# Kernel tuning notes

Hardware: AMD Instinct MI355X
Metric: run time of the kernel (lower is better)

## Reference

```python
import jax, jax.numpy as jnp
import numpy as np

EPS = 1e-5

def setup_inputs() -> dict:
    key = jax.random.key(0)
    ks = jax.random.split(key, 8)
    b, c, p, h = 8, 128, 2048, 4
    inp = {
        "input": jax.random.normal(ks[0], (b, c, p), jnp.float32),
        "gamma": jnp.ones((c,), jnp.float32),
        "beta": jnp.zeros((c,), jnp.float32),
        "Wq": jax.random.normal(ks[1], (c * h, c), jnp.float32) * (c ** -0.5),
        "bq": jnp.zeros((c * h,), jnp.float32),
        "Wk": jax.random.normal(ks[2], (c * h, c), jnp.float32) * (c ** -0.5),
        "bk": jnp.zeros((c * h,), jnp.float32),
        "Wv": jax.random.normal(ks[3], (c * h, c), jnp.float32) * (c ** -0.5),
        "bv": jnp.zeros((c * h,), jnp.float32),
        "Wo": jax.random.normal(ks[4], (c, c * h), jnp.float32) * ((c * h) ** -0.5),
        "bo": jnp.zeros((c,), jnp.float32),
    }
    return inp


def reference(input, gamma, beta, Wq, bq, Wk, bk, Wv, bv, Wo, bo):
    b, c, p = input.shape
    h = Wq.shape[0] // c
    # BatchNorm1d (training-mode batch stats): mean/var per channel over (batch, points)
    mean = jnp.mean(input, axis=(0, 2), keepdims=True)          # [1,c,1]
    var = jnp.mean((input - mean) ** 2, axis=(0, 2), keepdims=True)
    x = (input - mean) * jax.lax.rsqrt(var + EPS)
    x = x * gamma[None, :, None] + beta[None, :, None]
    # 1x1 conv projections == channel matmuls; then split c*h -> (c, h)
    q = (jnp.einsum('oc,bcp->bop', Wq, x) + bq[None, :, None]).reshape(b, c, h, p)
    k = (jnp.einsum('oc,bcp->bop', Wk, x) + bk[None, :, None]).reshape(b, c, h, p)
    v = (jnp.einsum('oc,bcp->bop', Wv, x) + bv[None, :, None]).reshape(b, c, h, p)
    # attention over points; scale by c**-0.5
    weight = jnp.einsum('bchi,bchj->bhij', q, k) * (c ** -0.5)   # [b,h,p,p]
    weight = jax.nn.softmax(weight, axis=3)
    att = jnp.einsum('bhij,bchj->bchi', weight, v)               # [b,c,h,p]
    att = att.reshape(b, c * h, p)
    out = jnp.einsum('oc,bcp->bop', Wo, att) + bo[None, :, None]
    return out + input
```

## Files before the change

### kernel.cpp

```cpp
#include <hip/hip_runtime.h>
#include <hip/hip_bf16.h>

#define NB 8
#define NC 128
#define NP 2048
#define NH 4
#define NCH 512

typedef __attribute__((ext_vector_type(8))) short bf16x8;
typedef __attribute__((ext_vector_type(16))) float f32x16;

__device__ __forceinline__ float bf2f(unsigned short u) {
  return __uint_as_float(((unsigned)u) << 16);
}
__device__ __forceinline__ unsigned short f2bf(float f) {
  __hip_bfloat16 h = __float2bfloat16(f);
  return *reinterpret_cast<unsigned short*>(&h);
}
__device__ __forceinline__ unsigned pk2(float lo, float hi) {
  return (unsigned)f2bf(lo) | ((unsigned)f2bf(hi) << 16);
}
__device__ __forceinline__ void gload_lds16(const void* g, void* l) {
  __builtin_amdgcn_global_load_lds(
      (const __attribute__((address_space(1))) void*)g,
      (__attribute__((address_space(3))) void*)l, 16, 0, 0);
}
__device__ __forceinline__ void plswap(unsigned& a, unsigned& b) {
  asm volatile("v_permlane32_swap_b32 %0, %1" : "+v"(a), "+v"(b));
}

__global__ __launch_bounds__(256) void bn_partial(
    const float* __restrict__ in, float* __restrict__ psum,
    float* __restrict__ psum2) {
  int c = blockIdx.x >> 2, qtr = blockIdx.x & 3;
  int t = threadIdx.x;
  float s = 0.f, s2 = 0.f;
  for (int b = 0; b < NB; ++b) {
    const float* ptr = in + ((size_t)b * NC + c) * NP + qtr * 512;
    #pragma unroll
    for (int p = 0; p < 2; ++p) {
      float v = ptr[p * 256 + t];
      s += v; s2 += v * v;
    }
  }
  for (int off = 32; off; off >>= 1) {
    s += __shfl_down(s, off, 64);
    s2 += __shfl_down(s2, off, 64);
  }
  __shared__ float red[8];
  int lane = t & 63, wid = t >> 6;
  if (!lane) { red[wid] = s; red[wid + 4] = s2; }
  __syncthreads();
  if (!t) {
    psum[blockIdx.x] = red[0] + red[1] + red[2] + red[3];
    psum2[blockIdx.x] = red[4] + red[5] + red[6] + red[7];
  }
}

__global__ __launch_bounds__(512, 2) void qkv_proj(
    const float* __restrict__ in, const float* __restrict__ gamma,
    const float* __restrict__ beta, const float* __restrict__ psum,
    const float* __restrict__ psum2, const float* __restrict__ Wq,
    const float* __restrict__ bq, const float* __restrict__ Wk,
    const float* __restrict__ bk, const float* __restrict__ Wv,
    const float* __restrict__ bv, unsigned short* __restrict__ qws,
    unsigned short* __restrict__ kws, unsigned short* __restrict__ vws) {
  __shared__ float sc[128], sh[128], bias[1536];
  __shared__ __align__(16) unsigned short Xt[64][136];
  int t = threadIdx.x;
  int pt = blockIdx.x & 31, b = blockIdx.x >> 5;
  int p0 = pt * 64;
  if (t < 128) {
    float s = psum[t * 4] + psum[t * 4 + 1] + psum[t * 4 + 2] + psum[t * 4 + 3];
    float s2 = psum2[t * 4] + psum2[t * 4 + 1] + psum2[t * 4 + 2] + psum2[t * 4 + 3];
    const float invn = 1.f / (NB * NP);
    float mean = s * invn, var = s2 * invn - mean * mean;
    float scl = gamma[t] * rsqrtf(var + 1e-5f);
    sc[t] = scl; sh[t] = beta[t] - mean * scl;
  }
  bias[t] = bq[t]; bias[512 + t] = bk[t]; bias[1024 + t] = bv[t];
  __syncthreads();
  {
    int p = t & 63, c0 = (t >> 6) * 16;
    const float* src = in + ((size_t)b * NC + c0) * NP + p0 + p;
    #pragma unroll
    for (int cc = 0; cc < 16; ++cc) {
      float v = src[(size_t)cc * NP];
      Xt[p][c0 + cc] = f2bf(v * sc[c0 + cc] + sh[c0 + cc]);
    }
  }
  __syncthreads();
  int w = t >> 6, lane = t & 63, l31 = lane & 31, h5 = lane >> 5;
  #pragma unroll 1
  for (int s = 0; s < 3; ++s) {
    int strip = s * 8 + w;
    int proj = strip >> 3, within = (strip & 7) * 64;
    const float* W = proj == 0 ? Wq : (proj == 1 ? Wk : Wv);
    f32x16 acc[2][2] = {};
    #pragma unroll
    for (int ks = 0; ks < 8; ++ks) {
      bf16x8 af[2], bf[2];
      #pragma unroll
      for (int mt = 0; mt < 2; ++mt) {
        const float* wr = W + (size_t)(within + mt * 32 + l31) * NC + ks * 16 + h5 * 8;
        float4 a = *(const float4*)wr, b4 = *(const float4*)(wr + 4);
        union { bf16x8 v; unsigned u[4]; } uu;
        uu.u[0] = pk2(a.x, a.y); uu.u[1] = pk2(a.z, a.w);
        uu.u[2] = pk2(b4.x, b4.y); uu.u[3] = pk2(b4.z, b4.w);
        af[mt] = uu.v;
      }
      #pragma unroll
      for (int nt = 0; nt < 2; ++nt)
        bf[nt] = *(const bf16x8*)&Xt[nt * 32 + l31][ks * 16 + h5 * 8];
      if (proj < 2) {
        #pragma unroll
        for (int mt = 0; mt < 2; ++mt)
          #pragma unroll
          for (int nt = 0; nt < 2; ++nt)
            acc[mt][nt] = __builtin_amdgcn_mfma_f32_32x32x16_bf16(bf[nt], af[mt], acc[mt][nt], 0, 0, 0);
      } else {
        #pragma unroll
        for (int mt = 0; mt < 2; ++mt)
          #pragma unroll
          for (int nt = 0; nt < 2; ++nt)
            acc[mt][nt] = __builtin_amdgcn_mfma_f32_32x32x16_bf16(af[mt], bf[nt], acc[mt][nt], 0, 0, 0);
      }
    }
    if (proj < 2) {
      unsigned short* dst = proj == 0 ? qws : kws;
      float qs = proj == 0 ? 0.12751743762765621f : 1.0f;
      #pragma unroll
      for (int mt = 0; mt < 2; ++mt) {
        int o = within + mt * 32 + l31;
        float bs = bias[proj * 512 + o];
        unsigned short* drow = dst + ((size_t)(b * 4 + (o & 3)) * NP) * NC + (o >> 2);
        #pragma unroll
        for (int nt = 0; nt < 2; ++nt)
          #pragma unroll
          for (int r = 0; r < 16; ++r) {
            int p = p0 + nt * 32 + (r & 3) + 8 * (r >> 2) + 4 * h5;
            drow[(size_t)p * NC] = f2bf((acc[mt][nt][r] + bs) * qs);
          }
      }
    } else {
      #pragma unroll
      for (int mt = 0; mt < 2; ++mt)
        #pragma unroll
        for (int nt = 0; nt < 2; ++nt)
          #pragma unroll
          for (int r = 0; r < 16; ++r) {
            int oo = within + mt * 32 + (r & 3) + 8 * (r >> 2) + 4 * h5;
            float val = acc[mt][nt][r] + bias[1024 + oo];
            vws[((size_t)(b * NCH + oo)) * NP + p0 + nt * 32 + l31] = f2bf(val);
          }
    }
  }
}

__global__ __launch_bounds__(256, 2) void attn(
    const unsigned short* __restrict__ qT, const unsigned short* __restrict__ kT,
    const unsigned short* __restrict__ vws, unsigned short* __restrict__ attws) {
  __shared__ uint4 Kbuf[2][1024];
  __shared__ uint4 Vbuf[2][1024];
  int tid = threadIdx.x;
  int wl = tid >> 6, lane = tid & 63, l31 = lane & 31, h5 = lane >> 5;
  int bid = blockIdx.x;
  int head = bid & 31, it = bid >> 5;
  int b = head >> 2, hh = head & 3;
  int i0 = it * 128;
  const unsigned short* krow = kT + (size_t)(b * 4 + hh) * NP * NC;
  const unsigned short* vb = vws + (size_t)b * NCH * NP;

  int t4 = tid >> 4;
  int ch = (tid & 15) ^ (t4 & 15);
  size_t vO = ((size_t)((t4 * 2 + (ch >> 3)) * 4 + hh)) * NP + (ch & 7) * 8;

  auto stage = [&](int bi, int j0v) {
    #pragma unroll
    for (int k = 0; k < 4; ++k) {
      gload_lds16(krow + (size_t)(j0v + k * 16 + t4) * NC + (ch << 3),
                  &Kbuf[bi][k * 256 + tid]);
      gload_lds16(vb + vO + (size_t)k * 128 * NP + j0v,
                  &Vbuf[bi][k * 256 + tid]);
    }
  };

  bf16x8 qf[8];
  {
    const unsigned short* qp =
        qT + ((size_t)(b * 4 + hh) * NP + (i0 + wl * 32 + l31)) * NC + h5 * 8;
    #pragma unroll
    for (int ks = 0; ks < 8; ++ks) qf[ks] = *(const bf16x8*)(qp + ks * 16);
  }

  f32x16 oacc[4] = {};
  float lsum = 0.f;

  stage(0, 0);
  __syncthreads();

  int kbase = l31 * 16, ksw = l31 & 15;
  #pragma unroll 1
  for (int tI = 0; tI < 32; ++tI) {
    int cur = tI & 1;
    if (tI < 31) stage(cur ^ 1, (tI + 1) * 64);

    f32x16 sacT0 = {}, sacT1 = {};
    #pragma unroll
    for (int ks = 0; ks < 8; ++ks) {
      int cidx = (ks * 2 + h5) ^ ksw;
      bf16x8 kf0 = *(const bf16x8*)&Kbuf[cur][kbase + cidx];
      bf16x8 kf1 = *(const bf16x8*)&Kbuf[cur][512 + kbase + cidx];
      sacT0 = __builtin_amdgcn_mfma_f32_32x32x16_bf16(kf0, qf[ks], sacT0, 0, 0, 0);
      sacT1 = __builtin_amdgcn_mfma_f32_32x32x16_bf16(kf1, qf[ks], sacT1, 0, 0, 0);
    }
    bf16x8 pfrag[4];
    #pragma unroll
    for (int ntj = 0; ntj < 2; ++ntj) {
      f32x16& sacT = ntj ? sacT1 : sacT0;
      #pragma unroll
      for (int r = 0; r < 16; ++r) {
        sacT[r] = __builtin_amdgcn_exp2f(sacT[r]);
        lsum += sacT[r];
      }
      unsigned wv[8];
      #pragma unroll
      for (int q = 0; q < 8; ++q) wv[q] = pk2(sacT[q * 2], sacT[q * 2 + 1]);
      plswap(wv[0], wv[2]); plswap(wv[1], wv[3]);
      plswap(wv[4], wv[6]); plswap(wv[5], wv[7]);
      union { bf16x8 v; unsigned u[4]; } f0, f1;
      f0.u[0] = wv[0]; f0.u[1] = wv[1]; f0.u[2] = wv[2]; f0.u[3] = wv[3];
      f1.u[0] = wv[4]; f1.u[1] = wv[5]; f1.u[2] = wv[6]; f1.u[3] = wv[7];
      pfrag[ntj * 2] = f0.v; pfrag[ntj * 2 + 1] = f1.v;
    }
    #pragma unroll
    for (int ntc = 0; ntc < 4; ++ntc) {
      int r = ntc * 16 + (l31 >> 1);
      int rb = r * 16, r15 = r & 15, c8 = (l31 & 1) * 8;
      #pragma unroll
      for (int kw = 0; kw < 4; ++kw) {
        bf16x8 vf = *(const bf16x8*)&Vbuf[cur][rb + ((c8 + kw * 2 + h5) ^ r15)];
        oacc[ntc] = __builtin_amdgcn_mfma_f32_32x32x16_bf16(vf, pfrag[kw], oacc[ntc], 0, 0, 0);
      }
    }
    __syncthreads();
  }

  float linv = 1.0f / (lsum + __shfl_xor(lsum, 32, 64));
  int i = i0 + wl * 32 + l31;
  #pragma unroll
  for (int ntc = 0; ntc < 4; ++ntc)
    #pragma unroll
    for (int r = 0; r < 16; ++r) {
      int c = ntc * 32 + (r & 3) + 8 * (r >> 2) + 4 * h5;
      attws[((size_t)(b * NCH + c * 4 + hh)) * NP + i] = f2bf(oacc[ntc][r] * linv);
    }
}

__global__ __launch_bounds__(256) void out_proj(
    const unsigned short* __restrict__ attws, const float* __restrict__ Wo,
    const float* __restrict__ bo, const float* __restrict__ in,
    float* __restrict__ out) {
  __shared__ __align__(16) unsigned short Xt[64][136];
  int t = threadIdx.x;
  int pt = blockIdx.x & 31, b = blockIdx.x >> 5;
  int p0 = pt * 64;
  int w = t >> 6, lane = t & 63, l31 = lane & 31, h5 = lane >> 5;
  f32x16 acc[2] = {};
  #pragma unroll 1
  for (int k0 = 0; k0 < 4; ++k0) {
    __syncthreads();
    {
      int k = t >> 1, ph = t & 1;
      const unsigned short* src = attws + ((size_t)(b * NCH + k0 * 128 + k)) * NP + p0 + ph * 32;
      union { int4 v[4]; unsigned short u[32]; } uu;
      uu.v[0] = *(const int4*)src;        uu.v[1] = *(const int4*)(src + 8);
      uu.v[2] = *(const int4*)(src + 16); uu.v[3] = *(const int4*)(src + 24);
      #pragma unroll
      for (int e = 0; e < 32; ++e) Xt[ph * 32 + e][k] = uu.u[e];
    }
    __syncthreads();
    #pragma unroll
    for (int ks = 0; ks < 8; ++ks) {
      const float* wr = Wo + (size_t)(w * 32 + l31) * NCH + k0 * 128 + ks * 16 + h5 * 8;
      float4 a = *(const float4*)wr, b4 = *(const float4*)(wr + 4);
      union { bf16x8 v; unsigned u[4]; } uu;
      uu.u[0] = pk2(a.x, a.y); uu.u[1] = pk2(a.z, a.w);
      uu.u[2] = pk2(b4.x, b4.y); uu.u[3] = pk2(b4.z, b4.w);
      #pragma unroll
      for (int nt = 0; nt < 2; ++nt) {
        bf16x8 bf = *(const bf16x8*)&Xt[nt * 32 + l31][ks * 16 + h5 * 8];
        acc[nt] = __builtin_amdgcn_mfma_f32_32x32x16_bf16(uu.v, bf, acc[nt], 0, 0, 0);
      }
    }
  }
  #pragma unroll
  for (int nt = 0; nt < 2; ++nt)
    #pragma unroll
    for (int r = 0; r < 16; ++r) {
      int o = w * 32 + (r & 3) + 8 * (r >> 2) + 4 * h5;
      int p = p0 + nt * 32 + l31;
      size_t idx = ((size_t)(b * NC + o)) * NP + p;
      out[idx] = acc[nt][r] + bo[o] + in[idx];
    }
}

extern "C" void kernel_launch(void* const* d_in, const int* in_sizes, int n_in,
                              void* d_out, int out_size, void* d_ws, size_t ws_size,
                              hipStream_t stream) {
  const float* in    = (const float*)d_in[0];
  const float* gamma = (const float*)d_in[1];
  const float* beta  = (const float*)d_in[2];
  const float* Wq = (const float*)d_in[3];
  const float* bq = (const float*)d_in[4];
  const float* Wk = (const float*)d_in[5];
  const float* bk = (const float*)d_in[6];
  const float* Wv = (const float*)d_in[7];
  const float* bv = (const float*)d_in[8];
  const float* Wo = (const float*)d_in[9];
  const float* bo = (const float*)d_in[10];
  float* out = (float*)d_out;

  char* ws = (char*)d_ws;
  float* psum  = (float*)ws;
  float* psum2 = psum + 512;
  const size_t QKV_ELEMS = (size_t)NB * NCH * NP;
  unsigned short* qws   = (unsigned short*)(ws + 8192);
  unsigned short* kws   = qws + QKV_ELEMS;
  unsigned short* vws   = kws + QKV_ELEMS;
  unsigned short* attws = vws + QKV_ELEMS;

  bn_partial<<<dim3(512), dim3(256), 0, stream>>>(in, psum, psum2);
  qkv_proj<<<dim3(256), dim3(512), 0, stream>>>(
      in, gamma, beta, psum, psum2, Wq, bq, Wk, bk, Wv, bv, qws, kws, vws);
  attn<<<dim3(512), dim3(256), 0, stream>>>(qws, kws, vws, attws);
  out_proj<<<dim3(256), dim3(256), 0, stream>>>(attws, Wo, bo, in, out);
}
```

Before: 204.4 us.

## Give each attention wave two query tiles, halving block size to 128 threads

The attention kernel now runs 2 waves per block instead of 4, and each wave handles 64 query rows as two 32-row tiles. Each K and V fragment read from LDS then feeds two MFMAs, which halves LDS reads per unit of compute. Staging is recomputed with precomputed per-thread pointers for the 128-thread layout. The cost is many more registers (two sets of Q fragments, score tiles and output accumulators), with launch bounds set to 128 threads and 1 block, which may lower occupancy and latency hiding.

Measured after the change: 224.3 us. +9.8%, slower.

```diff
diff --git a/kernel.cpp b/kernel.cpp
--- a/kernel.cpp
+++ b/kernel.cpp
@@ -157,7 +157,7 @@
   }
 }
 
-__global__ __launch_bounds__(256, 2) void attn(
+__global__ __launch_bounds__(128, 1) void attn(
     const unsigned short* __restrict__ qT, const unsigned short* __restrict__ kT,
     const unsigned short* __restrict__ vws, unsigned short* __restrict__ attws) {
   __shared__ uint4 Kbuf[2][1024];
@@ -171,30 +171,35 @@
   const unsigned short* krow = kT + (size_t)(b * 4 + hh) * NP * NC;
   const unsigned short* vb = vws + (size_t)b * NCH * NP;
 
-  int t4 = tid >> 4;
-  int ch = (tid & 15) ^ (t4 & 15);
-  size_t vO = ((size_t)((t4 * 2 + (ch >> 3)) * 4 + hh)) * NP + (ch & 7) * 8;
-
+  int t16 = tid >> 4;
+  const unsigned short* kpt[8];
+  const unsigned short* vpt[8];
+  #pragma unroll
+  for (int k = 0; k < 8; ++k) {
+    int row = k * 8 + t16;
+    int chk = (tid & 15) ^ (row & 15);
+    kpt[k] = krow + (size_t)row * NC + (chk << 3);
+    vpt[k] = vb + ((size_t)((row * 2 + (chk >> 3)) * 4 + hh)) * NP + ((chk & 7) << 3);
+  }
   auto stage = [&](int bi, int j0v) {
     #pragma unroll
-    for (int k = 0; k < 4; ++k) {
-      gload_lds16(krow + (size_t)(j0v + k * 16 + t4) * NC + (ch << 3),
-                  &Kbuf[bi][k * 256 + tid]);
-      gload_lds16(vb + vO + (size_t)k * 128 * NP + j0v,
-                  &Vbuf[bi][k * 256 + tid]);
+    for (int k = 0; k < 8; ++k) {
+      gload_lds16(kpt[k] + (size_t)j0v * NC, &Kbuf[bi][k * 128 + tid]);
+      gload_lds16(vpt[k] + j0v, &Vbuf[bi][k * 128 + tid]);
     }
   };
 
-  bf16x8 qf[8];
-  {
+  bf16x8 qf[2][8];
+  #pragma unroll
+  for (int is = 0; is < 2; ++is) {
     const unsigned short* qp =
-        qT + ((size_t)(b * 4 + hh) * NP + (i0 + wl * 32 + l31)) * NC + h5 * 8;
-    #pragma unroll
-    for (int ks = 0; ks < 8; ++ks) qf[ks] = *(const bf16x8*)(qp + ks * 16);
-  }
-
-  f32x16 oacc[4] = {};
-  float lsum = 0.f;
+        qT + ((size_t)(b * 4 + hh) * NP + (i0 + wl * 64 + is * 32 + l31)) * NC + h5 * 8;
+    #pragma unroll
+    for (int ks = 0; ks < 8; ++ks) qf[is][ks] = *(const bf16x8*)(qp + ks * 16);
+  }
+
+  f32x16 oacc[2][4] = {};
+  float lsum0 = 0.f, lsum1 = 0.f;
 
   stage(0, 0);
   __syncthreads();
@@ -205,24 +210,28 @@
     int cur = tI & 1;
     if (tI < 31) stage(cur ^ 1, (tI + 1) * 64);
 
-    f32x16 sacT0 = {}, sacT1 = {};
+    f32x16 sac00 = {}, sac01 = {}, sac10 = {}, sac11 = {};
     #pragma unroll
     for (int ks = 0; ks < 8; ++ks) {
       int cidx = (ks * 2 + h5) ^ ksw;
       bf16x8 kf0 = *(const bf16x8*)&Kbuf[cur][kbase + cidx];
       bf16x8 kf1 = *(const bf16x8*)&Kbuf[cur][512 + kbase + cidx];
-      sacT0 = __builtin_amdgcn_mfma_f32_32x32x16_bf16(kf0, qf[ks], sacT0, 0, 0, 0);
-      sacT1 = __builtin_amdgcn_mfma_f32_32x32x16_bf16(kf1, qf[ks], sacT1, 0, 0, 0);
-    }
-    bf16x8 pfrag[4];
-    #pragma unroll
-    for (int ntj = 0; ntj < 2; ++ntj) {
-      f32x16& sacT = ntj ? sacT1 : sacT0;
+      sac00 = __builtin_amdgcn_mfma_f32_32x32x16_bf16(kf0, qf[0][ks], sac00, 0, 0, 0);
+      sac01 = __builtin_amdgcn_mfma_f32_32x32x16_bf16(kf1, qf[0][ks], sac01, 0, 0, 0);
+      sac10 = __builtin_amdgcn_mfma_f32_32x32x16_bf16(kf0, qf[1][ks], sac10, 0, 0, 0);
+      sac11 = __builtin_amdgcn_mfma_f32_32x32x16_bf16(kf1, qf[1][ks], sac11, 0, 0, 0);
+    }
+    bf16x8 pfrag0[4], pfrag1[4];
+    #pragma unroll
+    for (int sel = 0; sel < 4; ++sel) {
+      f32x16& sacT = sel == 0 ? sac00 : (sel == 1 ? sac01 : (sel == 2 ? sac10 : sac11));
+      float ls = 0.f;
       #pragma unroll
       for (int r = 0; r < 16; ++r) {
         sacT[r] = __builtin_amdgcn_exp2f(sacT[r]);
-        lsum += sacT[r];
-      }
+        ls += sacT[r];
+      }
+      if (sel < 2) lsum0 += ls; else lsum1 += ls;
       unsigned wv[8];
       #pragma unroll
       for (int q = 0; q < 8; ++q) wv[q] = pk2(sacT[q * 2], sacT[q * 2 + 1]);
@@ -231,7 +240,9 @@
       union { bf16x8 v; unsigned u[4]; } f0, f1;
       f0.u[0] = wv[0]; f0.u[1] = wv[1]; f0.u[2] = wv[2]; f0.u[3] = wv[3];
       f1.u[0] = wv[4]; f1.u[1] = wv[5]; f1.u[2] = wv[6]; f1.u[3] = wv[7];
-      pfrag[ntj * 2] = f0.v; pfrag[ntj * 2 + 1] = f1.v;
+      int ntj = sel & 1;
+      if (sel < 2) { pfrag0[ntj * 2] = f0.v; pfrag0[ntj * 2 + 1] = f1.v; }
+      else         { pfrag1[ntj * 2] = f0.v; pfrag1[ntj * 2 + 1] = f1.v; }
     }
     #pragma unroll
     for (int ntc = 0; ntc < 4; ++ntc) {
@@ -240,21 +251,27 @@
       #pragma unroll
       for (int kw = 0; kw < 4; ++kw) {
         bf16x8 vf = *(const bf16x8*)&Vbuf[cur][rb + ((c8 + kw * 2 + h5) ^ r15)];
-        oacc[ntc] = __builtin_amdgcn_mfma_f32_32x32x16_bf16(vf, pfrag[kw], oacc[ntc], 0, 0, 0);
+        oacc[0][ntc] = __builtin_amdgcn_mfma_f32_32x32x16_bf16(vf, pfrag0[kw], oacc[0][ntc], 0, 0, 0);
+        oacc[1][ntc] = __builtin_amdgcn_mfma_f32_32x32x16_bf16(vf, pfrag1[kw], oacc[1][ntc], 0, 0, 0);
       }
     }
     __syncthreads();
   }
 
-  float linv = 1.0f / (lsum + __shfl_xor(lsum, 32, 64));
-  int i = i0 + wl * 32 + l31;
+  float linv0 = 1.0f / (lsum0 + __shfl_xor(lsum0, 32, 64));
+  float linv1 = 1.0f / (lsum1 + __shfl_xor(lsum1, 32, 64));
   #pragma unroll
-  for (int ntc = 0; ntc < 4; ++ntc)
-    #pragma unroll
-    for (int r = 0; r < 16; ++r) {
-      int c = ntc * 32 + (r & 3) + 8 * (r >> 2) + 4 * h5;
-      attws[((size_t)(b * NCH + c * 4 + hh)) * NP + i] = f2bf(oacc[ntc][r] * linv);
-    }
+  for (int is = 0; is < 2; ++is) {
+    float linv = is == 0 ? linv0 : linv1;
+    int i = i0 + wl * 64 + is * 32 + l31;
+    #pragma unroll
+    for (int ntc = 0; ntc < 4; ++ntc)
+      #pragma unroll
+      for (int r = 0; r < 16; ++r) {
+        int c = ntc * 32 + (r & 3) + 8 * (r >> 2) + 4 * h5;
+        attws[((size_t)(b * NCH + c * 4 + hh)) * NP + i] = f2bf(oacc[is][ntc][r] * linv);
+      }
+  }
 }
 
 __global__ __launch_bounds__(256) void out_proj(
@@ -333,6 +350,6 @@
   bn_partial<<<dim3(512), dim3(256), 0, stream>>>(in, psum, psum2);
   qkv_proj<<<dim3(256), dim3(512), 0, stream>>>(
       in, gamma, beta, psum, psum2, Wq, bq, Wk, bk, Wv, bv, qws, kws, vws);
-  attn<<<dim3(512), dim3(256), 0, stream>>>(qws, kws, vws, attws);
+  attn<<<dim3(512), dim3(128), 0, stream>>>(qws, kws, vws, attws);
   out_proj<<<dim3(256), dim3(256), 0, stream>>>(attws, Wo, bo, in, out);
 }
```

## Store attention output point-major and double-buffer out_proj loads via LDS DMA

Applied to the files above, without the earlier changes.

The attention kernel now writes its output in [b, p, c*h] order instead of [b, c*h, p]. This lets out_proj stage each 32-point tile with direct global-to-LDS 16-byte loads into an XOR-swizzled layout, replacing the per-element transpose through shared memory. The staging is double-buffered across the four k-chunks, the tile shrinks to 32 points, and the grid doubles to 512 blocks with a launch bound of 2 blocks per CU. The cost is that attn's output stores now have a large stride across c, so those writes scatter and may coalesce poorly.

New measurement: 224.4 us. 9.8% more time.

```diff
diff --git a/kernel.cpp b/kernel.cpp
--- a/kernel.cpp
+++ b/kernel.cpp
@@ -253,33 +253,37 @@
     #pragma unroll
     for (int r = 0; r < 16; ++r) {
       int c = ntc * 32 + (r & 3) + 8 * (r >> 2) + 4 * h5;
-      attws[((size_t)(b * NCH + c * 4 + hh)) * NP + i] = f2bf(oacc[ntc][r] * linv);
-    }
-}
-
-__global__ __launch_bounds__(256) void out_proj(
-    const unsigned short* __restrict__ attws, const float* __restrict__ Wo,
+      attws[((size_t)(b * NP + i)) * NCH + c * 4 + hh] = f2bf(oacc[ntc][r] * linv);
+    }
+}
+
+__global__ __launch_bounds__(256, 2) void out_proj(
+    const unsigned short* __restrict__ attT, const float* __restrict__ Wo,
     const float* __restrict__ bo, const float* __restrict__ in,
     float* __restrict__ out) {
-  __shared__ __align__(16) unsigned short Xt[64][136];
+  __shared__ uint4 Abuf[2][512];
   int t = threadIdx.x;
-  int pt = blockIdx.x & 31, b = blockIdx.x >> 5;
-  int p0 = pt * 64;
+  int pt = blockIdx.x & 63, b = blockIdx.x >> 6;
+  int p0 = pt * 32;
   int w = t >> 6, lane = t & 63, l31 = lane & 31, h5 = lane >> 5;
-  f32x16 acc[2] = {};
+  const unsigned short* ab = attT + (size_t)b * NP * NCH;
+  int row0 = t >> 4, pos = t & 15;
+  auto stage = [&](int bi, int k0) {
+    #pragma unroll
+    for (int q = 0; q < 2; ++q) {
+      int row = q * 16 + row0;
+      int chq = pos ^ (row & 15);
+      gload_lds16(ab + ((size_t)(p0 + row)) * NCH + k0 * 128 + chq * 8,
+                  &Abuf[bi][q * 256 + t]);
+    }
+  };
+  f32x16 acc = {};
+  stage(0, 0);
+  __syncthreads();
   #pragma unroll 1
   for (int k0 = 0; k0 < 4; ++k0) {
-    __syncthreads();
-    {
-      int k = t >> 1, ph = t & 1;
-      const unsigned short* src = attws + ((size_t)(b * NCH + k0 * 128 + k)) * NP + p0 + ph * 32;
-      union { int4 v[4]; unsigned short u[32]; } uu;
-      uu.v[0] = *(const int4*)src;        uu.v[1] = *(const int4*)(src + 8);
-      uu.v[2] = *(const int4*)(src + 16); uu.v[3] = *(const int4*)(src + 24);
-      #pragma unroll
-      for (int e = 0; e < 32; ++e) Xt[ph * 32 + e][k] = uu.u[e];
-    }
-    __syncthreads();
+    int cur = k0 & 1;
+    if (k0 < 3) stage(cur ^ 1, k0 + 1);
     #pragma unroll
     for (int ks = 0; ks < 8; ++ks) {
       const float* wr = Wo + (size_t)(w * 32 + l31) * NCH + k0 * 128 + ks * 16 + h5 * 8;
@@ -287,22 +291,18 @@
       union { bf16x8 v; unsigned u[4]; } uu;
       uu.u[0] = pk2(a.x, a.y); uu.u[1] = pk2(a.z, a.w);
       uu.u[2] = pk2(b4.x, b4.y); uu.u[3] = pk2(b4.z, b4.w);
-      #pragma unroll
-      for (int nt = 0; nt < 2; ++nt) {
-        bf16x8 bf = *(const bf16x8*)&Xt[nt * 32 + l31][ks * 16 + h5 * 8];
-        acc[nt] = __builtin_amdgcn_mfma_f32_32x32x16_bf16(uu.v, bf, acc[nt], 0, 0, 0);
-      }
-    }
+      bf16x8 bf = *(const bf16x8*)&Abuf[cur][l31 * 16 + ((ks * 2 + h5) ^ (l31 & 15))];
+      acc = __builtin_amdgcn_mfma_f32_32x32x16_bf16(uu.v, bf, acc, 0, 0, 0);
+    }
+    __syncthreads();
   }
   #pragma unroll
-  for (int nt = 0; nt < 2; ++nt)
-    #pragma unroll
-    for (int r = 0; r < 16; ++r) {
-      int o = w * 32 + (r & 3) + 8 * (r >> 2) + 4 * h5;
-      int p = p0 + nt * 32 + l31;
-      size_t idx = ((size_t)(b * NC + o)) * NP + p;
-      out[idx] = acc[nt][r] + bo[o] + in[idx];
-    }
+  for (int r = 0; r < 16; ++r) {
+    int o = w * 32 + (r & 3) + 8 * (r >> 2) + 4 * h5;
+    int p = p0 + l31;
+    size_t idx = ((size_t)(b * NC + o)) * NP + p;
+    out[idx] = acc[r] + bo[o] + in[idx];
+  }
 }
 
 extern "C" void kernel_launch(void* const* d_in, const int* in_sizes, int n_in,
@@ -334,5 +334,5 @@
   qkv_proj<<<dim3(256), dim3(512), 0, stream>>>(
       in, gamma, beta, psum, psum2, Wq, bq, Wk, bk, Wv, bv, qws, kws, vws);
   attn<<<dim3(512), dim3(256), 0, stream>>>(qws, kws, vws, attws);
-  out_proj<<<dim3(256), dim3(256), 0, stream>>>(attws, Wo, bo, in, out);
-}
+  out_proj<<<dim3(512), dim3(256), 0, stream>>>(attws, Wo, bo, in, out);
+}
```
